# Performance work log

Measured on AMD Instinct MI355X. Metric: run time of the kernel, lower is better.

## Reference

```python
import jax, jax.numpy as jnp
import numpy as np

DIM = 256
NUM_ITERS = 5
NUM_CLASSES = 365
TRIU_LEN = DIM * (DIM + 1) // 2  # 32896

# lower-triangular (incl. diag) flat indices in row-major order, matching
# torch.ones(d,d).triu().t().reshape(-1).nonzero()
_TRIL_IDX = np.nonzero(np.tril(np.ones((DIM, DIM), np.bool_)).reshape(-1))[0]


def setup_inputs() -> dict:
    key = jax.random.key(0)
    k1, k2 = jax.random.split(key)
    B = 64
    x = jax.random.normal(k1, (B, DIM, 14, 14), dtype=jnp.float32)
    fc_w = jax.random.normal(k2, (NUM_CLASSES, TRIU_LEN), dtype=jnp.float32) * 0.01
    fc_b = jnp.zeros((NUM_CLASSES,), dtype=jnp.float32)
    return {"x": x, "fc_w": fc_w, "fc_b": fc_b}


def _cov(x):
    # x: [B, D, H, W] -> centered second-order pooling [B, D, D]
    B, D, H, W = x.shape
    M = H * W
    xf = x.reshape(B, D, M)
    xc = xf - jnp.mean(xf, axis=2, keepdims=True)
    # x @ I_hat @ x^T == (xc @ xf^T) / M == (xc @ xc^T) / M
    y = jnp.einsum('bdm,bem->bde', xc, xc) / M
    return y + 1e-7 * jnp.eye(D, dtype=x.dtype)


def _matrix_sqrt_ns(a, num_iters):
    # Newton-Schulz iteration for matrix square root; a: [B, D, D]
    B, D, _ = a.shape
    I = jnp.eye(D, dtype=a.dtype)
    normA = jnp.trace(a, axis1=1, axis2=2)  # [B]
    Y = a / normA[:, None, None]
    Z = jnp.broadcast_to(I, (B, D, D))
    for _ in range(num_iters):
        T = 0.5 * (3.0 * I - jnp.einsum('bij,bjk->bik', Z, Y))
        Y = jnp.einsum('bij,bjk->bik', Y, T)
        Z = jnp.einsum('bij,bjk->bik', T, Z)
    return Y * jnp.sqrt(normA)[:, None, None]


def _triu(x):
    # gather lower-tri (== upper-tri of symmetric cov) entries: [B, D, D] -> [B, D(D+1)/2]
    B, D, _ = x.shape
    return x.reshape(B, D * D)[:, _TRIL_IDX]


def reference(x, fc_w, fc_b):
    y = _cov(x)
    y = _matrix_sqrt_ns(y, NUM_ITERS)
    y = _triu(y)
    return y @ fc_w.T + fc_b
```

## Files before the change

### kernel.cpp

```cpp
#include <hip/hip_runtime.h>
#include <hip/hip_bf16.h>

typedef __attribute__((ext_vector_type(8))) short bf16x8;
typedef __attribute__((ext_vector_type(4))) float f32x4;

static __device__ __forceinline__ ushort f2b(float f) {
    unsigned u = __float_as_uint(f);
    return (ushort)((u + 0x7fffu + ((u >> 16) & 1u)) >> 16);
}

static __device__ __forceinline__ void gload16(const void* g, void* lds) {
    __builtin_amdgcn_global_load_lds(
        (const __attribute__((address_space(1))) unsigned int*)g,
        (__attribute__((address_space(3))) unsigned int*)lds, 16, 0, 0);
}

__global__ __launch_bounds__(256) void prep_kernel(
    const float* __restrict__ x, ushort* __restrict__ xc, float* __restrict__ var)
{
    const int t = threadIdx.x, wv = t >> 6, l = t & 63;
    const int bid = blockIdx.x;
    const int x8 = bid & 7, rr = bid >> 3;
    const int dgrp = rr & 63, bgrp = rr >> 6;
    const int b = bgrp * 8 + x8;
    const int rowid = b * 256 + dgrp * 4 + wv;
    const float* xr = x + (size_t)rowid * 196;

    float x0 = xr[l];
    float x1 = xr[l + 64];
    float x2 = xr[l + 128];
    float x3 = (l < 4) ? xr[l + 192] : 0.0f;

    float s1 = x0 + x1 + x2 + x3;
    float s2 = x0*x0 + x1*x1 + x2*x2 + x3*x3;
    #pragma unroll
    for (int off = 32; off; off >>= 1) {
        s1 += __shfl_xor(s1, off);
        s2 += __shfl_xor(s2, off);
    }
    const float mean = s1 * (1.0f / 196.0f);
    if (l == 0) var[rowid] = s2 * (1.0f / 196.0f) - mean * mean + 1e-7f;

    ushort* xcr = xc + (size_t)rowid * 256;
    xcr[l]       = f2b(x0 - mean);
    xcr[l + 64]  = f2b(x1 - mean);
    xcr[l + 128] = f2b(x2 - mean);
    xcr[l + 192] = (l < 4) ? f2b(x3 - mean) : (ushort)0;
}

template<int H>
static __device__ __forceinline__ void stage_half(
    const ushort* Ab, const ushort* Btb, int i0, int j0,
    int wv, int lrow, int seg, ushort* As, ushort* Bs)
{
    #pragma unroll
    for (int it = 0; it < 8; ++it) {
        const int c = H * 32 + wv * 8 + it;
        const int tk = c >> 3, r16 = c & 7;
        const int row = r16 * 16 + lrow;
        gload16(Ab + (size_t)(i0 + row) * 256 + tk * 32 + seg,
                (char*)As + tk * 8192 + r16 * 1024);
        gload16(Btb + (size_t)(j0 + row) * 256 + tk * 32 + seg,
                (char*)Bs + tk * 8192 + r16 * 1024);
    }
}

template<int MODE>
__global__ __launch_bounds__(256) void gemm_ns(
    const ushort* __restrict__ A, const ushort* __restrict__ A2,
    const ushort* __restrict__ Bt,
    ushort* __restrict__ C, ushort* __restrict__ C2,
    const float* __restrict__ var)
{
    __shared__ ushort As[8][128][32];
    __shared__ ushort Bs[8][128][32];
    __shared__ float tr_s[4];

    const int bid = blockIdx.x, x8 = bid & 7;
    int b, i0, j0;
    bool useA2 = false;
    if (MODE == 2) {
        const int tt = (bid >> 3) & 3;
        useA2 = ((bid >> 5) & 1) != 0;
        b = (bid >> 6) * 8 + x8;
        i0 = (tt >> 1) * 128; j0 = (tt & 1) * 128;
    } else if (MODE == 3) {
        const int rr = bid >> 3, t3 = rr % 3;
        b = (rr / 3) * 8 + x8;
        i0 = (t3 == 0) ? 0 : 128;
        j0 = (t3 == 2) ? 128 : 0;
    } else {
        const int tt = (bid >> 3) & 3;
        b = (bid >> 5) * 8 + x8;
        i0 = (tt >> 1) * 128; j0 = (tt & 1) * 128;
    }
    const ushort* Ab  = (useA2 ? A2 : A) + (size_t)b * 65536;
    const ushort* Btb = Bt + (size_t)b * 65536;

    const int t = threadIdx.x, wv = t >> 6, l = t & 63;
    const int li = l & 15, hi = l >> 4;
    const int wr = wv >> 1, wc = wv & 1;
    const int lrow = l >> 2;
    const int seg = (l & 3) * 8;

    stage_half<0>(Ab, Btb, i0, j0, wv, lrow, seg, &As[0][0][0], &Bs[0][0][0]);

    if (MODE == 0 || MODE == 3) {
        float v = var[b * 256 + t];
        #pragma unroll
        for (int off = 32; off; off >>= 1) v += __shfl_xor(v, off);
        if (l == 0) tr_s[wv] = v;
    }
    __syncthreads();
    float trace = 0.f;
    if (MODE == 0 || MODE == 3) trace = tr_s[0] + tr_s[1] + tr_s[2] + tr_s[3];

    f32x4 acc[4][4];
    #pragma unroll
    for (int m = 0; m < 4; ++m)
        #pragma unroll
        for (int n = 0; n < 4; ++n) acc[m][n] = (f32x4){0.f, 0.f, 0.f, 0.f};

    stage_half<1>(Ab, Btb, i0, j0, wv, lrow, seg, &As[0][0][0], &Bs[0][0][0]);

    #pragma unroll
    for (int tk = 0; tk < 4; ++tk) {
        bf16x8 af[4], bfr[4];
        #pragma unroll
        for (int m = 0; m < 4; ++m)
            af[m] = *(const bf16x8*)&As[tk][wr * 64 + m * 16 + li][hi * 8];
        #pragma unroll
        for (int n = 0; n < 4; ++n)
            bfr[n] = *(const bf16x8*)&Bs[tk][wc * 64 + n * 16 + li][hi * 8];
        #pragma unroll
        for (int m = 0; m < 4; ++m)
            #pragma unroll
            for (int n = 0; n < 4; ++n)
                acc[m][n] = __builtin_amdgcn_mfma_f32_16x16x32_bf16(
                    af[m], bfr[n], acc[m][n], 0, 0, 0);
    }
    __syncthreads();
    #pragma unroll
    for (int tk = 4; tk < 8; ++tk) {
        bf16x8 af[4], bfr[4];
        #pragma unroll
        for (int m = 0; m < 4; ++m)
            af[m] = *(const bf16x8*)&As[tk][wr * 64 + m * 16 + li][hi * 8];
        #pragma unroll
        for (int n = 0; n < 4; ++n)
            bfr[n] = *(const bf16x8*)&Bs[tk][wc * 64 + n * 16 + li][hi * 8];
        #pragma unroll
        for (int m = 0; m < 4; ++m)
            #pragma unroll
            for (int n = 0; n < 4; ++n)
                acc[m][n] = __builtin_amdgcn_mfma_f32_16x16x32_bf16(
                    af[m], bfr[n], acc[m][n], 0, 0, 0);
    }

    if (MODE == 3) {
        const float sc = sqrtf(trace);
        ushort* trib = C + (size_t)b * 32896;
        #pragma unroll
        for (int m = 0; m < 4; ++m)
            #pragma unroll
            for (int n = 0; n < 4; ++n)
                #pragma unroll
                for (int r = 0; r < 4; ++r) {
                    const int gi = i0 + wr * 64 + m * 16 + hi * 4 + r;
                    const int gj = j0 + wc * 64 + n * 16 + li;
                    if (gj <= gi)
                        trib[(gi * (gi + 1)) / 2 + gj] = f2b(acc[m][n][r] * sc);
                }
    } else {
        const float invtr = (MODE == 0) ? (1.0f / trace) : 0.0f;
        ushort* Cb  = ((MODE == 2 && useA2) ? C2 : C) + (size_t)b * 65536;
        ushort* C2b = (MODE == 0) ? (C2 + (size_t)b * 65536) : nullptr;
        #pragma unroll
        for (int m = 0; m < 4; ++m)
            #pragma unroll
            for (int n = 0; n < 4; ++n)
                #pragma unroll
                for (int r = 0; r < 4; ++r) {
                    const int gi = i0 + wr * 64 + m * 16 + hi * 4 + r;
                    const int gj = j0 + wc * 64 + n * 16 + li;
                    const float v = acc[m][n][r];
                    const size_t idx = (size_t)gi * 256 + gj;
                    if (MODE == 0) {
                        float y0 = (v * (1.0f / 196.0f) + ((gi == gj) ? 1e-7f : 0.0f)) * invtr;
                        Cb[idx]  = f2b(y0);
                        C2b[idx] = f2b(((gi == gj) ? 1.5f : 0.0f) - 0.5f * y0);
                    } else if (MODE == 1) {
                        Cb[idx] = f2b(((gi == gj) ? 1.5f : 0.0f) - 0.5f * v);
                    } else {
                        Cb[idx] = f2b(v);
                    }
                }
    }
}

__global__ __launch_bounds__(256) void fc_gemm(
    const ushort* __restrict__ tri, const float* __restrict__ W,
    float* __restrict__ partial)
{
    __shared__ ushort Asl[4][64][32];
    __shared__ float  Wsl[4][64][32];

    const int ntile = blockIdx.x;
    const int split = blockIdx.y;
    const int steps = 16 + (split < 4 ? 1 : 0);
    const int step0 = split * 16 + (split < 4 ? split : 4);

    const int tid = threadIdx.x, wv = tid >> 6, l = tid & 63;
    const int li = l & 15, hi = l >> 4;

    const int arow = tid >> 2, aseg = tid & 3;
    const int wrow0 = tid >> 3, wseg = tid & 7;
    const int wrow1 = 32 + (tid >> 3);
    const int wcl0 = min(ntile * 64 + wrow0, 364);
    const int wcl1 = min(ntile * 64 + wrow1, 364);

#define FSTAGE(s) do {                                                          \
    const int kk_ = (step0 + (s)) * 32;                                         \
    const int r_ = (s) & 3;                                                     \
    gload16(tri + (size_t)arow * 32896 + kk_ + aseg * 8,                        \
            &Asl[r_][arow][aseg * 8]);                                          \
    gload16(W + (size_t)wcl0 * 32896 + kk_ + wseg * 4,                          \
            &Wsl[r_][wrow0][wseg * 4]);                                         \
    gload16(W + (size_t)wcl1 * 32896 + kk_ + wseg * 4,                          \
            &Wsl[r_][wrow1][wseg * 4]);                                         \
} while (0)

    FSTAGE(0); FSTAGE(1); FSTAGE(2);

    f32x4 acc[4];
    #pragma unroll
    for (int m = 0; m < 4; ++m) acc[m] = (f32x4){0.f, 0.f, 0.f, 0.f};

    for (int s = 0; s < steps; ++s) {
        if (s + 3 < steps) FSTAGE(s + 3);
        asm volatile("s_waitcnt vmcnt(9)" ::: "memory");
        __builtin_amdgcn_sched_barrier(0);
        __builtin_amdgcn_s_barrier();

        const int r = s & 3;
        const float4 wf0 = *(const float4*)&Wsl[r][wv * 16 + li][hi * 8];
        const float4 wf1 = *(const float4*)&Wsl[r][wv * 16 + li][hi * 8 + 4];
        bf16x8 bfr;
        bfr[0] = (short)f2b(wf0.x); bfr[1] = (short)f2b(wf0.y);
        bfr[2] = (short)f2b(wf0.z); bfr[3] = (short)f2b(wf0.w);
        bfr[4] = (short)f2b(wf1.x); bfr[5] = (short)f2b(wf1.y);
        bfr[6] = (short)f2b(wf1.z); bfr[7] = (short)f2b(wf1.w);

        bf16x8 af[4];
        #pragma unroll
        for (int m = 0; m < 4; ++m)
            af[m] = *(const bf16x8*)&Asl[r][m * 16 + li][hi * 8];
        #pragma unroll
        for (int m = 0; m < 4; ++m)
            acc[m] = __builtin_amdgcn_mfma_f32_16x16x32_bf16(af[m], bfr, acc[m], 0, 0, 0);

        __builtin_amdgcn_s_barrier();
    }
#undef FSTAGE

    #pragma unroll
    for (int m = 0; m < 4; ++m)
        #pragma unroll
        for (int rr = 0; rr < 4; ++rr) {
            const int i = m * 16 + hi * 4 + rr;
            const int j = ntile * 64 + wv * 16 + li;
            partial[((size_t)split * 64 + i) * 384 + j] = acc[m][rr];
        }
}

__global__ void fc_reduce(const float* __restrict__ partial,
                          const float* __restrict__ bias, float* __restrict__ out)
{
    const int idx = blockIdx.x * 256 + threadIdx.x;
    if (idx >= 64 * 365) return;
    const int b = idx / 365, n = idx % 365;
    float s = bias[n];
    #pragma unroll 4
    for (int sp = 0; sp < 64; ++sp)
        s += partial[((size_t)sp * 64 + b) * 384 + n];
    out[idx] = s;
}

extern "C" void kernel_launch(void* const* d_in, const int* in_sizes, int n_in,
                              void* d_out, int out_size, void* d_ws, size_t ws_size,
                              hipStream_t stream)
{
    (void)in_sizes; (void)n_in; (void)out_size; (void)ws_size;
    const float* x   = (const float*)d_in[0];
    const float* fcw = (const float*)d_in[1];
    const float* fcb = (const float*)d_in[2];
    float* out = (float*)d_out;
    char* ws = (char*)d_ws;

    const size_t MS = (size_t)64 * 256 * 256 * 2;
    ushort* w0 = (ushort*)(ws + 0 * MS);
    ushort* w1 = (ushort*)(ws + 1 * MS);
    ushort* w2 = (ushort*)(ws + 2 * MS);
    ushort* w3 = (ushort*)(ws + 3 * MS);
    ushort* w4 = (ushort*)(ws + 4 * MS);
    ushort* xc = (ushort*)(ws + 5 * MS);
    float*  var    = (float*)(ws + 6 * MS);
    ushort* tri    = (ushort*)(ws + 6 * MS + 131072);
    float*  partial= (float*)(ws + 6 * MS + 131072 + 4210688);

    prep_kernel<<<4096, 256, 0, stream>>>(x, xc, var);

    gemm_ns<0><<<256, 256, 0, stream>>>(xc, nullptr, xc, w0, w1, var);
    gemm_ns<4><<<256, 256, 0, stream>>>(w0, nullptr, w1, w2, nullptr, nullptr);
    gemm_ns<1><<<256, 256, 0, stream>>>(w1, nullptr, w2, w0, nullptr, nullptr);
    gemm_ns<2><<<512, 256, 0, stream>>>(w2, w1, w0, w3, w4, nullptr);
    gemm_ns<1><<<256, 256, 0, stream>>>(w4, nullptr, w3, w0, nullptr, nullptr);
    gemm_ns<2><<<512, 256, 0, stream>>>(w3, w4, w0, w1, w2, nullptr);
    gemm_ns<1><<<256, 256, 0, stream>>>(w2, nullptr, w1, w0, nullptr, nullptr);
    gemm_ns<2><<<512, 256, 0, stream>>>(w1, w2, w0, w3, w4, nullptr);
    gemm_ns<1><<<256, 256, 0, stream>>>(w4, nullptr, w3, w0, nullptr, nullptr);
    gemm_ns<3><<<192, 256, 0, stream>>>(w3, nullptr, w0, tri, nullptr, var);

    fc_gemm<<<dim3(6, 64), 256, 0, stream>>>(tri, fcw, partial);
    fc_reduce<<<(64 * 365 + 255) / 256, 256, 0, stream>>>(partial, fcb, out);
}
```

Baseline: 122.8 us.

## Fuse Newton-Schulz T computation with Y/Z update in one kernel per iteration

Each Newton-Schulz iteration used to be two launches: one computing T = 1.5I - 0.5·Z·Y into global memory, and one computing Y·T and T·Z. These are merged into a single ns_fused kernel. Each block recomputes the 128-row (or column) panel of T it needs, keeps it in LDS, then multiplies it with the staged Y or Z panel. This removes launches and the global round trip of T, at the cost of duplicated T computation across blocks and extra LDS staging. The FC split-K is also raised from 64 to 85 splits, with the reduction kernel adjusted to match.

```diff
diff --git a/kernel.cpp b/kernel.cpp
--- a/kernel.cpp
+++ b/kernel.cpp
@@ -48,27 +48,49 @@
     xcr[l + 192] = (l < 4) ? f2b(x3 - mean) : (ushort)0;
 }
 
-template<int H>
-static __device__ __forceinline__ void stage_half(
-    const ushort* Ab, const ushort* Btb, int i0, int j0,
-    int wv, int lrow, int seg, ushort* As, ushort* Bs)
-{
-    #pragma unroll
-    for (int it = 0; it < 8; ++it) {
-        const int c = H * 32 + wv * 8 + it;
+static __device__ __forceinline__ void stage_panel(
+    const ushort* __restrict__ rows, void* panel, int wv, int l)
+{
+    const int lrow = l >> 2;
+    const int seg = (l & 3) * 8;
+    #pragma unroll
+    for (int it = 0; it < 16; ++it) {
+        const int c = wv * 16 + it;
         const int tk = c >> 3, r16 = c & 7;
         const int row = r16 * 16 + lrow;
-        gload16(Ab + (size_t)(i0 + row) * 256 + tk * 32 + seg,
-                (char*)As + tk * 8192 + r16 * 1024);
-        gload16(Btb + (size_t)(j0 + row) * 256 + tk * 32 + seg,
-                (char*)Bs + tk * 8192 + r16 * 1024);
-    }
-}
+        gload16(rows + (size_t)row * 256 + tk * 32 + seg,
+                (char*)panel + tk * 8192 + r16 * 1024);
+    }
+}
+
+static __device__ __forceinline__ void compute_tile(
+    const ushort (&Ap)[8][128][32], const ushort (&Bp)[8][128][32],
+    f32x4 (&acc)[4][4], int wr, int wc, int li, int hi)
+{
+    #pragma unroll
+    for (int tk = 0; tk < 8; ++tk) {
+        bf16x8 af[4], bfr[4];
+        #pragma unroll
+        for (int m = 0; m < 4; ++m)
+            af[m] = *(const bf16x8*)&Ap[tk][wr * 64 + m * 16 + li][hi * 8];
+        #pragma unroll
+        for (int n = 0; n < 4; ++n)
+            bfr[n] = *(const bf16x8*)&Bp[tk][wc * 64 + n * 16 + li][hi * 8];
+        #pragma unroll
+        for (int m = 0; m < 4; ++m)
+            #pragma unroll
+            for (int n = 0; n < 4; ++n)
+                acc[m][n] = __builtin_amdgcn_mfma_f32_16x16x32_bf16(
+                    af[m], bfr[n], acc[m][n], 0, 0, 0);
+    }
+}
+
+#define ZERO4x4(a) do { _Pragma("unroll") for (int m_ = 0; m_ < 4; ++m_) \
+    _Pragma("unroll") for (int n_ = 0; n_ < 4; ++n_) a[m_][n_] = (f32x4){0.f,0.f,0.f,0.f}; } while (0)
 
 template<int MODE>
 __global__ __launch_bounds__(256) void gemm_ns(
-    const ushort* __restrict__ A, const ushort* __restrict__ A2,
-    const ushort* __restrict__ Bt,
+    const ushort* __restrict__ A, const ushort* __restrict__ Bt,
     ushort* __restrict__ C, ushort* __restrict__ C2,
     const float* __restrict__ var)
 {
@@ -77,35 +99,20 @@
     __shared__ float tr_s[4];
 
     const int bid = blockIdx.x, x8 = bid & 7;
-    int b, i0, j0;
-    bool useA2 = false;
-    if (MODE == 2) {
-        const int tt = (bid >> 3) & 3;
-        useA2 = ((bid >> 5) & 1) != 0;
-        b = (bid >> 6) * 8 + x8;
-        i0 = (tt >> 1) * 128; j0 = (tt & 1) * 128;
-    } else if (MODE == 3) {
-        const int rr = bid >> 3, t3 = rr % 3;
-        b = (rr / 3) * 8 + x8;
-        i0 = (t3 == 0) ? 0 : 128;
-        j0 = (t3 == 2) ? 128 : 0;
-    } else {
-        const int tt = (bid >> 3) & 3;
-        b = (bid >> 5) * 8 + x8;
-        i0 = (tt >> 1) * 128; j0 = (tt & 1) * 128;
-    }
-    const ushort* Ab  = (useA2 ? A2 : A) + (size_t)b * 65536;
+    const int tt = (bid >> 3) & 3;
+    const int b = (bid >> 5) * 8 + x8;
+    const int i0 = (tt >> 1) * 128, j0 = (tt & 1) * 128;
+    const ushort* Ab  = A  + (size_t)b * 65536;
     const ushort* Btb = Bt + (size_t)b * 65536;
 
     const int t = threadIdx.x, wv = t >> 6, l = t & 63;
     const int li = l & 15, hi = l >> 4;
     const int wr = wv >> 1, wc = wv & 1;
-    const int lrow = l >> 2;
-    const int seg = (l & 3) * 8;
-
-    stage_half<0>(Ab, Btb, i0, j0, wv, lrow, seg, &As[0][0][0], &Bs[0][0][0]);
-
-    if (MODE == 0 || MODE == 3) {
+
+    stage_panel(Ab  + (size_t)i0 * 256, As, wv, l);
+    stage_panel(Btb + (size_t)j0 * 256, Bs, wv, l);
+
+    if (MODE == 0) {
         float v = var[b * 256 + t];
         #pragma unroll
         for (int off = 32; off; off >>= 1) v += __shfl_xor(v, off);
@@ -113,53 +120,118 @@
     }
     __syncthreads();
     float trace = 0.f;
-    if (MODE == 0 || MODE == 3) trace = tr_s[0] + tr_s[1] + tr_s[2] + tr_s[3];
+    if (MODE == 0) trace = tr_s[0] + tr_s[1] + tr_s[2] + tr_s[3];
 
     f32x4 acc[4][4];
+    ZERO4x4(acc);
+    compute_tile(As, Bs, acc, wr, wc, li, hi);
+
+    const float invtr = (MODE == 0) ? (1.0f / trace) : 0.0f;
+    ushort* Cb  = C + (size_t)b * 65536;
+    ushort* C2b = (MODE == 0) ? (C2 + (size_t)b * 65536) : nullptr;
     #pragma unroll
     for (int m = 0; m < 4; ++m)
         #pragma unroll
-        for (int n = 0; n < 4; ++n) acc[m][n] = (f32x4){0.f, 0.f, 0.f, 0.f};
-
-    stage_half<1>(Ab, Btb, i0, j0, wv, lrow, seg, &As[0][0][0], &Bs[0][0][0]);
-
-    #pragma unroll
-    for (int tk = 0; tk < 4; ++tk) {
-        bf16x8 af[4], bfr[4];
-        #pragma unroll
-        for (int m = 0; m < 4; ++m)
-            af[m] = *(const bf16x8*)&As[tk][wr * 64 + m * 16 + li][hi * 8];
-        #pragma unroll
         for (int n = 0; n < 4; ++n)
-            bfr[n] = *(const bf16x8*)&Bs[tk][wc * 64 + n * 16 + li][hi * 8];
-        #pragma unroll
-        for (int m = 0; m < 4; ++m)
-            #pragma unroll
-            for (int n = 0; n < 4; ++n)
-                acc[m][n] = __builtin_amdgcn_mfma_f32_16x16x32_bf16(
-                    af[m], bfr[n], acc[m][n], 0, 0, 0);
-    }
-    __syncthreads();
-    #pragma unroll
-    for (int tk = 4; tk < 8; ++tk) {
-        bf16x8 af[4], bfr[4];
-        #pragma unroll
-        for (int m = 0; m < 4; ++m)
-            af[m] = *(const bf16x8*)&As[tk][wr * 64 + m * 16 + li][hi * 8];
+            #pragma unroll
+            for (int r = 0; r < 4; ++r) {
+                const int gi = i0 + wr * 64 + m * 16 + hi * 4 + r;
+                const int gj = j0 + wc * 64 + n * 16 + li;
+                const float v = acc[m][n][r];
+                const size_t idx = (size_t)gi * 256 + gj;
+                if (MODE == 0) {
+                    float y0 = (v * (1.0f / 196.0f) + ((gi == gj) ? 1e-7f : 0.0f)) * invtr;
+                    Cb[idx]  = f2b(y0);
+                    C2b[idx] = f2b(((gi == gj) ? 1.5f : 0.0f) - 0.5f * y0);
+                } else {
+                    Cb[idx] = f2b(v);
+                }
+            }
+}
+
+template<bool FINAL>
+__global__ __launch_bounds__(256) void ns_fused(
+    const ushort* __restrict__ Y, const ushort* __restrict__ Z,
+    ushort* __restrict__ Yo, ushort* __restrict__ Zo,
+    const float* __restrict__ var)
+{
+    __shared__ ushort As[8][128][32];
+    __shared__ ushort Bs[8][128][32];
+    __shared__ float tr_s[4];
+
+    const int bid = blockIdx.x, x8 = bid & 7;
+    int b, i0, j0;
+    bool isZ = false;
+    if (FINAL) {
+        const int rr = bid >> 3, role = rr % 3;
+        b = (rr / 3) * 8 + x8;
+        i0 = (role == 0) ? 0 : 128;
+        j0 = (role == 2) ? 128 : 0;
+    } else {
+        const int role = (bid >> 3) & 7;
+        b = (bid >> 6) * 8 + x8;
+        isZ = role >= 4;
+        const int t4 = role & 3;
+        i0 = (t4 >> 1) * 128;
+        j0 = (t4 & 1) * 128;
+    }
+    const int p = isZ ? i0 : j0;
+    const size_t bo = (size_t)b * 65536;
+    const ushort* Yb = Y + bo;
+    const ushort* Zb = Z + bo;
+
+    const int tid = threadIdx.x, wv = tid >> 6, l = tid & 63;
+    const int li = l & 15, hi = l >> 4, wr = wv >> 1, wc = wv & 1;
+
+    stage_panel(Zb + (size_t)p * 256, As, wv, l);
+    stage_panel(Yb, Bs, wv, l);
+    if (FINAL) {
+        float v = var[b * 256 + tid];
+        #pragma unroll
+        for (int off = 32; off; off >>= 1) v += __shfl_xor(v, off);
+        if (l == 0) tr_s[wv] = v;
+    }
+    __syncthreads();
+    float sc = 0.f;
+    if (FINAL) sc = sqrtf(tr_s[0] + tr_s[1] + tr_s[2] + tr_s[3]);
+
+    f32x4 t0a[4][4], t1a[4][4];
+    ZERO4x4(t0a);
+    compute_tile(As, Bs, t0a, wr, wc, li, hi);
+    __syncthreads();
+    stage_panel(Yb + 128 * 256, Bs, wv, l);
+    __syncthreads();
+    ZERO4x4(t1a);
+    compute_tile(As, Bs, t1a, wr, wc, li, hi);
+    __syncthreads();
+
+    const bool keepBs = (!isZ) && (i0 == 128);
+    if (!keepBs)
+        stage_panel((isZ ? Zb + (size_t)j0 * 256 : Yb + (size_t)i0 * 256), Bs, wv, l);
+
+    #pragma unroll
+    for (int m = 0; m < 4; ++m)
         #pragma unroll
         for (int n = 0; n < 4; ++n)
-            bfr[n] = *(const bf16x8*)&Bs[tk][wc * 64 + n * 16 + li][hi * 8];
-        #pragma unroll
-        for (int m = 0; m < 4; ++m)
-            #pragma unroll
-            for (int n = 0; n < 4; ++n)
-                acc[m][n] = __builtin_amdgcn_mfma_f32_16x16x32_bf16(
-                    af[m], bfr[n], acc[m][n], 0, 0, 0);
-    }
-
-    if (MODE == 3) {
-        const float sc = sqrtf(trace);
-        ushort* trib = C + (size_t)b * 32896;
+            #pragma unroll
+            for (int r = 0; r < 4; ++r) {
+                const int gi = wr * 64 + m * 16 + hi * 4 + r;
+                const int gj = wc * 64 + n * 16 + li;
+                const float v0 = ((p + gi) == gj ? 1.5f : 0.0f) - 0.5f * t0a[m][n][r];
+                As[gj >> 5][gi][gj & 31] = f2b(v0);
+                const int gj1 = 128 + gj;
+                const float v1 = ((p + gi) == gj1 ? 1.5f : 0.0f) - 0.5f * t1a[m][n][r];
+                As[gj1 >> 5][gi][gj1 & 31] = f2b(v1);
+            }
+    __syncthreads();
+
+    f32x4 oacc[4][4];
+    ZERO4x4(oacc);
+    if (isZ) compute_tile(As, Bs, oacc, wr, wc, li, hi);
+    else     compute_tile(Bs, As, oacc, wr, wc, li, hi);
+
+    if (FINAL) {
+        ushort* trib = Yo + (size_t)b * 32896;
         #pragma unroll
         for (int m = 0; m < 4; ++m)
             #pragma unroll
@@ -169,12 +241,10 @@
                     const int gi = i0 + wr * 64 + m * 16 + hi * 4 + r;
                     const int gj = j0 + wc * 64 + n * 16 + li;
                     if (gj <= gi)
-                        trib[(gi * (gi + 1)) / 2 + gj] = f2b(acc[m][n][r] * sc);
+                        trib[(gi * (gi + 1)) / 2 + gj] = f2b(oacc[m][n][r] * sc);
                 }
     } else {
-        const float invtr = (MODE == 0) ? (1.0f / trace) : 0.0f;
-        ushort* Cb  = ((MODE == 2 && useA2) ? C2 : C) + (size_t)b * 65536;
-        ushort* C2b = (MODE == 0) ? (C2 + (size_t)b * 65536) : nullptr;
+        ushort* Ob = (isZ ? Zo : Yo) + bo;
         #pragma unroll
         for (int m = 0; m < 4; ++m)
             #pragma unroll
@@ -183,17 +253,7 @@
                 for (int r = 0; r < 4; ++r) {
                     const int gi = i0 + wr * 64 + m * 16 + hi * 4 + r;
                     const int gj = j0 + wc * 64 + n * 16 + li;
-                    const float v = acc[m][n][r];
-                    const size_t idx = (size_t)gi * 256 + gj;
-                    if (MODE == 0) {
-                        float y0 = (v * (1.0f / 196.0f) + ((gi == gj) ? 1e-7f : 0.0f)) * invtr;
-                        Cb[idx]  = f2b(y0);
-                        C2b[idx] = f2b(((gi == gj) ? 1.5f : 0.0f) - 0.5f * y0);
-                    } else if (MODE == 1) {
-                        Cb[idx] = f2b(((gi == gj) ? 1.5f : 0.0f) - 0.5f * v);
-                    } else {
-                        Cb[idx] = f2b(v);
-                    }
+                    Ob[(size_t)gi * 256 + gj] = f2b(oacc[m][n][r]);
                 }
     }
 }
@@ -207,8 +267,8 @@
 
     const int ntile = blockIdx.x;
     const int split = blockIdx.y;
-    const int steps = 16 + (split < 4 ? 1 : 0);
-    const int step0 = split * 16 + (split < 4 ? split : 4);
+    const int steps = 12 + (split < 8 ? 1 : 0);
+    const int step0 = split * 12 + (split < 8 ? split : 8);
 
     const int tid = threadIdx.x, wv = tid >> 6, l = tid & 63;
     const int li = l & 15, hi = l >> 4;
@@ -280,8 +340,8 @@
     if (idx >= 64 * 365) return;
     const int b = idx / 365, n = idx % 365;
     float s = bias[n];
-    #pragma unroll 4
-    for (int sp = 0; sp < 64; ++sp)
+    #pragma unroll 5
+    for (int sp = 0; sp < 85; ++sp)
         s += partial[((size_t)sp * 64 + b) * 384 + n];
     out[idx] = s;
 }
@@ -310,17 +370,13 @@
 
     prep_kernel<<<4096, 256, 0, stream>>>(x, xc, var);
 
-    gemm_ns<0><<<256, 256, 0, stream>>>(xc, nullptr, xc, w0, w1, var);
-    gemm_ns<4><<<256, 256, 0, stream>>>(w0, nullptr, w1, w2, nullptr, nullptr);
-    gemm_ns<1><<<256, 256, 0, stream>>>(w1, nullptr, w2, w0, nullptr, nullptr);
-    gemm_ns<2><<<512, 256, 0, stream>>>(w2, w1, w0, w3, w4, nullptr);
-    gemm_ns<1><<<256, 256, 0, stream>>>(w4, nullptr, w3, w0, nullptr, nullptr);
-    gemm_ns<2><<<512, 256, 0, stream>>>(w3, w4, w0, w1, w2, nullptr);
-    gemm_ns<1><<<256, 256, 0, stream>>>(w2, nullptr, w1, w0, nullptr, nullptr);
-    gemm_ns<2><<<512, 256, 0, stream>>>(w1, w2, w0, w3, w4, nullptr);
-    gemm_ns<1><<<256, 256, 0, stream>>>(w4, nullptr, w3, w0, nullptr, nullptr);
-    gemm_ns<3><<<192, 256, 0, stream>>>(w3, nullptr, w0, tri, nullptr, var);
-
-    fc_gemm<<<dim3(6, 64), 256, 0, stream>>>(tri, fcw, partial);
+    gemm_ns<0><<<256, 256, 0, stream>>>(xc, xc, w0, w1, var);
+    gemm_ns<4><<<256, 256, 0, stream>>>(w0, w1, w2, nullptr, nullptr);
+    ns_fused<false><<<512, 256, 0, stream>>>(w2, w1, w3, w4, nullptr);
+    ns_fused<false><<<512, 256, 0, stream>>>(w3, w4, w0, xc, nullptr);
+    ns_fused<false><<<512, 256, 0, stream>>>(w0, xc, w2, w1, nullptr);
+    ns_fused<true><<<192, 256, 0, stream>>>(w2, w1, tri, nullptr, var);
+
+    fc_gemm<<<dim3(6, 85), 256, 0, stream>>>(tri, fcw, partial);
     fc_reduce<<<(64 * 365 + 255) / 256, 256, 0, stream>>>(partial, fcb, out);
 }
```

Result: slower. 138.4 us (+12.7%).

## Double-buffer K-chunks in NS GEMM and widen FC split-K

Applied to the files above, without the earlier changes.

The Newton-Schulz GEMM previously staged the full K=256 panel into LDS in two halves. It now loads four 64-wide K chunks through a two-slot ring buffer, fetching the next chunk while MFMAs run on the current one. This halves LDS use per block and aims to overlap global-to-LDS loads with compute, at the cost of more barriers. Separately, the FC split-K count goes from 64 to 85 to launch more blocks, which makes the partial buffer and the reduction loop larger.

```diff
diff --git a/kernel.cpp b/kernel.cpp
--- a/kernel.cpp
+++ b/kernel.cpp
@@ -48,23 +48,6 @@
     xcr[l + 192] = (l < 4) ? f2b(x3 - mean) : (ushort)0;
 }
 
-template<int H>
-static __device__ __forceinline__ void stage_half(
-    const ushort* Ab, const ushort* Btb, int i0, int j0,
-    int wv, int lrow, int seg, ushort* As, ushort* Bs)
-{
-    #pragma unroll
-    for (int it = 0; it < 8; ++it) {
-        const int c = H * 32 + wv * 8 + it;
-        const int tk = c >> 3, r16 = c & 7;
-        const int row = r16 * 16 + lrow;
-        gload16(Ab + (size_t)(i0 + row) * 256 + tk * 32 + seg,
-                (char*)As + tk * 8192 + r16 * 1024);
-        gload16(Btb + (size_t)(j0 + row) * 256 + tk * 32 + seg,
-                (char*)Bs + tk * 8192 + r16 * 1024);
-    }
-}
-
 template<int MODE>
 __global__ __launch_bounds__(256) void gemm_ns(
     const ushort* __restrict__ A, const ushort* __restrict__ A2,
@@ -72,8 +55,8 @@
     ushort* __restrict__ C, ushort* __restrict__ C2,
     const float* __restrict__ var)
 {
-    __shared__ ushort As[8][128][32];
-    __shared__ ushort Bs[8][128][32];
+    __shared__ ushort As[2][2][128][32];
+    __shared__ ushort Bs[2][2][128][32];
     __shared__ float tr_s[4];
 
     const int bid = blockIdx.x, x8 = bid & 7;
@@ -103,8 +86,20 @@
     const int lrow = l >> 2;
     const int seg = (l & 3) * 8;
 
-    stage_half<0>(Ab, Btb, i0, j0, wv, lrow, seg, &As[0][0][0], &Bs[0][0][0]);
-
+#define STAGE(buf, ck) do {                                                     \
+    _Pragma("unroll")                                                           \
+    for (int it = 0; it < 4; ++it) {                                            \
+        const int c16 = wv * 4 + it;                                 \
+        const int tk = c16 >> 3, r16 = c16 & 7;                                 \
+        const int row = r16 * 16 + lrow;                                        \
+        gload16(Ab + (size_t)(i0 + row) * 256 + (ck) * 64 + tk * 32 + seg,      \
+                (char*)&As[buf][0][0][0] + tk * 8192 + r16 * 1024);             \
+        gload16(Btb + (size_t)(j0 + row) * 256 + (ck) * 64 + tk * 32 + seg,     \
+                (char*)&Bs[buf][0][0][0] + tk * 8192 + r16 * 1024);             \
+    }                                                                           \
+} while (0)
+
+    STAGE(0, 0);
     if (MODE == 0 || MODE == 3) {
         float v = var[b * 256 + t];
         #pragma unroll
@@ -121,41 +116,30 @@
         #pragma unroll
         for (int n = 0; n < 4; ++n) acc[m][n] = (f32x4){0.f, 0.f, 0.f, 0.f};
 
-    stage_half<1>(Ab, Btb, i0, j0, wv, lrow, seg, &As[0][0][0], &Bs[0][0][0]);
-
-    #pragma unroll
-    for (int tk = 0; tk < 4; ++tk) {
-        bf16x8 af[4], bfr[4];
-        #pragma unroll
-        for (int m = 0; m < 4; ++m)
-            af[m] = *(const bf16x8*)&As[tk][wr * 64 + m * 16 + li][hi * 8];
-        #pragma unroll
-        for (int n = 0; n < 4; ++n)
-            bfr[n] = *(const bf16x8*)&Bs[tk][wc * 64 + n * 16 + li][hi * 8];
-        #pragma unroll
-        for (int m = 0; m < 4; ++m)
+    int cur = 0;
+    #pragma unroll
+    for (int ck = 0; ck < 4; ++ck) {
+        if (ck < 3) STAGE(cur ^ 1, ck + 1);
+        #pragma unroll
+        for (int s = 0; s < 2; ++s) {
+            bf16x8 af[4], bfr[4];
+            #pragma unroll
+            for (int m = 0; m < 4; ++m)
+                af[m] = *(const bf16x8*)&As[cur][s][wr * 64 + m * 16 + li][hi * 8];
             #pragma unroll
             for (int n = 0; n < 4; ++n)
-                acc[m][n] = __builtin_amdgcn_mfma_f32_16x16x32_bf16(
-                    af[m], bfr[n], acc[m][n], 0, 0, 0);
-    }
-    __syncthreads();
-    #pragma unroll
-    for (int tk = 4; tk < 8; ++tk) {
-        bf16x8 af[4], bfr[4];
-        #pragma unroll
-        for (int m = 0; m < 4; ++m)
-            af[m] = *(const bf16x8*)&As[tk][wr * 64 + m * 16 + li][hi * 8];
-        #pragma unroll
-        for (int n = 0; n < 4; ++n)
-            bfr[n] = *(const bf16x8*)&Bs[tk][wc * 64 + n * 16 + li][hi * 8];
-        #pragma unroll
-        for (int m = 0; m < 4; ++m)
-            #pragma unroll
-            for (int n = 0; n < 4; ++n)
-                acc[m][n] = __builtin_amdgcn_mfma_f32_16x16x32_bf16(
-                    af[m], bfr[n], acc[m][n], 0, 0, 0);
-    }
+                bfr[n] = *(const bf16x8*)&Bs[cur][s][wc * 64 + n * 16 + li][hi * 8];
+            #pragma unroll
+            for (int m = 0; m < 4; ++m)
+                #pragma unroll
+                for (int n = 0; n < 4; ++n)
+                    acc[m][n] = __builtin_amdgcn_mfma_f32_16x16x32_bf16(
+                        af[m], bfr[n], acc[m][n], 0, 0, 0);
+        }
+        __syncthreads();
+        cur ^= 1;
+    }
+#undef STAGE
 
     if (MODE == 3) {
         const float sc = sqrtf(trace);
@@ -207,8 +191,8 @@
 
     const int ntile = blockIdx.x;
     const int split = blockIdx.y;
-    const int steps = 16 + (split < 4 ? 1 : 0);
-    const int step0 = split * 16 + (split < 4 ? split : 4);
+    const int steps = 12 + (split < 8 ? 1 : 0);
+    const int step0 = split * 12 + (split < 8 ? split : 8);
 
     const int tid = threadIdx.x, wv = tid >> 6, l = tid & 63;
     const int li = l & 15, hi = l >> 4;
@@ -280,8 +264,8 @@
     if (idx >= 64 * 365) return;
     const int b = idx / 365, n = idx % 365;
     float s = bias[n];
-    #pragma unroll 4
-    for (int sp = 0; sp < 64; ++sp)
+    #pragma unroll 5
+    for (int sp = 0; sp < 85; ++sp)
         s += partial[((size_t)sp * 64 + b) * 384 + n];
     out[idx] = s;
 }
@@ -321,6 +305,6 @@
     gemm_ns<1><<<256, 256, 0, stream>>>(w4, nullptr, w3, w0, nullptr, nullptr);
     gemm_ns<3><<<192, 256, 0, stream>>>(w3, nullptr, w0, tri, nullptr, var);
 
-    fc_gemm<<<dim3(6, 64), 256, 0, stream>>>(tri, fcw, partial);
+    fc_gemm<<<dim3(6, 85), 256, 0, stream>>>(tri, fcw, partial);
     fc_reduce<<<(64 * 365 + 255) / 256, 256, 0, stream>>>(partial, fcb, out);
 }
```

Result: faster. 115.1 us (-6.3%).
